# Optimization experiments

Hardware: AMD Instinct MI355X
Metric: run time of the kernel (lower is better)

The kernel has to match this reference:

```python
import jax, jax.numpy as jnp
import numpy as np

D_MODEL = 1024
NUM_HEADS = 16
HEAD_DIM = D_MODEL // NUM_HEADS


def setup_inputs() -> dict:
    key = jax.random.key(0)
    k1, k2, k3 = jax.random.split(key, 3)
    B, S = 2, 2048
    x = jax.random.normal(k1, (B, S, D_MODEL), dtype=jnp.float32)
    # torch nn.Linear weight layout: [out_features, in_features]
    qkv_w = jax.random.normal(k2, (3 * D_MODEL, D_MODEL), dtype=jnp.float32) * (D_MODEL ** -0.5)
    qkv_b = jnp.zeros((3 * D_MODEL,), dtype=jnp.float32)
    out_w = jax.random.normal(k3, (D_MODEL, D_MODEL), dtype=jnp.float32) * (D_MODEL ** -0.5)
    out_b = jnp.zeros((D_MODEL,), dtype=jnp.float32)
    return {"x": x, "qkv_w": qkv_w, "qkv_b": qkv_b, "out_w": out_w, "out_b": out_b}


def reference(x, qkv_w, qkv_b, out_w, out_b):
    B, S, D = x.shape
    H, hd = NUM_HEADS, HEAD_DIM
    # fused QKV projection (torch Linear: x @ W.T + b)
    qkv = jnp.dot(x, qkv_w.T) + qkv_b              # [B, S, 3D]
    qkv = qkv.reshape(B, S, 3, H, hd)
    qkv = jnp.transpose(qkv, (2, 0, 3, 1, 4))       # [3, B, H, S, hd]
    q, k, v = qkv[0], qkv[1], qkv[2]
    scale = hd ** -0.5
    scores = jnp.einsum('bhqd,bhkd->bhqk', q, k) * scale  # [B, H, S, S]
    # causal mask (TritonSoftmax(is_causal=True))
    causal = jnp.tril(jnp.ones((S, S), dtype=bool))
    scores = jnp.where(causal, scores, jnp.float32(-jnp.inf))
    attn = jax.nn.softmax(scores, axis=-1)
    ctx = jnp.einsum('bhqk,bhkd->bhqd', attn, v)    # [B, H, S, hd]
    ctx = jnp.transpose(ctx, (0, 2, 1, 3)).reshape(B, S, D)
    return jnp.dot(ctx, out_w.T) + out_b
```

## Files before the change

### kernel.cpp

```cpp
#include <hip/hip_runtime.h>

typedef unsigned short u16;
typedef __bf16 bf16x8 __attribute__((ext_vector_type(8)));
typedef float f32x4 __attribute__((ext_vector_type(4)));

#define LOG2E 1.44269504088896340736f

__device__ __forceinline__ u16 f2bf(float f) {
  unsigned int u = __builtin_bit_cast(unsigned int, f);
  u += 0x7FFFu + ((u >> 16) & 1u);
  return (u16)(u >> 16);
}

__device__ __forceinline__ unsigned int cvtpk_bf16(float lo, float hi) {
  unsigned int r;
  asm("v_cvt_pk_bf16_f32 %0, %1, %2" : "=v"(r) : "v"(lo), "v"(hi));
  return r;
}

__device__ __forceinline__ void async16(const void* g, void* l) {
  __builtin_amdgcn_global_load_lds((void*)g, (void*)l, 16, 0, 0);
}

__global__ void cast_all(const float* __restrict__ x, const float* __restrict__ w1,
                         const float* __restrict__ w2, u16* __restrict__ xb,
                         u16* __restrict__ w1b, u16* __restrict__ w2b) {
  int i = blockIdx.x * blockDim.x + threadIdx.x;
  const float* s; u16* d; int j;
  if (i < 1048576)      { s = x;  d = xb;  j = i; }
  else if (i < 1835008) { s = w1; d = w1b; j = i - 1048576; }
  else                  { s = w2; d = w2b; j = i - 1835008; }
  float4 v = ((const float4*)s)[j];
  union { u16 s4[4]; uint2 u; } o;
  o.s4[0] = f2bf(v.x); o.s4[1] = f2bf(v.y); o.s4[2] = f2bf(v.z); o.s4[3] = f2bf(v.w);
  ((uint2*)d)[j] = o.u;
}

template <int EPI, int BN>
__global__ __launch_bounds__(256)
void gemm_nt(const u16* __restrict__ A, const u16* __restrict__ Bw,
             int M, int N, int K, const float* __restrict__ bias,
             u16* __restrict__ qo, u16* __restrict__ ko, u16* __restrict__ vto,
             float* __restrict__ out, int ntn) {
  __shared__ __align__(16) u16 As[128 * 32];
  __shared__ __align__(16) u16 Bs[BN * 32];
  constexpr int JN = BN / 32;
  constexpr int NB = (BN * 4) / 256;
  const int tid = threadIdx.x;
  const int w = tid >> 6, lane = tid & 63;
  const int lr = lane & 15, lkb = lane >> 4;
  const int bx = blockIdx.x;
  const int mt = bx / ntn, nt = bx % ntn;
  const int m0 = mt * 128, n0 = nt * BN;
  const int wm = (w >> 1) * 64, wn = (w & 1) * (BN / 2);

  f32x4 acc[4][JN] = {};

  int srow[2], sgch[2];
#pragma unroll
  for (int i = 0; i < 2; ++i) {
    int cid = tid + i * 256;
    srow[i] = cid >> 2;
    sgch[i] = (cid & 3) ^ (srow[i] & 3);
  }

  for (int k0 = 0; k0 < K; k0 += 32) {
#pragma unroll
    for (int i = 0; i < 2; ++i) {
      char* la = (char*)As + (w * 64 + i * 256) * 16;
      async16(A + (size_t)(m0 + srow[i]) * K + k0 + sgch[i] * 8, la);
    }
#pragma unroll
    for (int i = 0; i < NB; ++i) {
      char* lb = (char*)Bs + (w * 64 + i * 256) * 16;
      async16(Bw + (size_t)(n0 + srow[i]) * K + k0 + sgch[i] * 8, lb);
    }
    __syncthreads();

    bf16x8 af[4], bfr[JN];
#pragma unroll
    for (int i = 0; i < 4; ++i) {
      int ra = wm + i * 16 + lr;
      af[i] = *(const bf16x8*)(As + ra * 32 + (lkb ^ (ra & 3)) * 8);
    }
#pragma unroll
    for (int j = 0; j < JN; ++j) {
      int rb = wn + j * 16 + lr;
      bfr[j] = *(const bf16x8*)(Bs + rb * 32 + (lkb ^ (rb & 3)) * 8);
    }
#pragma unroll
    for (int i = 0; i < 4; ++i)
#pragma unroll
      for (int j = 0; j < JN; ++j)
        acc[i][j] = __builtin_amdgcn_mfma_f32_16x16x32_bf16(af[i], bfr[j], acc[i][j], 0, 0, 0);
    __syncthreads();
  }

  if constexpr (EPI == 0) {
    const int which = n0 >> 10;
    const float qscale = (which == 0) ? 0.125f : 1.0f;
#pragma unroll
    for (int i = 0; i < 4; ++i) {
#pragma unroll
      for (int j = 0; j < JN; ++j) {
        int n = n0 + wn + j * 16 + lr;
        float bv = bias[n];
        int d = n & 1023, h = d >> 6, dd = d & 63;
#pragma unroll
        for (int r = 0; r < 4; ++r) {
          int m = m0 + wm + i * 16 + lkb * 4 + r;
          int b = m >> 11, s = m & 2047;
          int bh = b * 16 + h;
          u16 val = f2bf((acc[i][j][r] + bv) * qscale);
          if (which == 0)      qo[(bh * 2048 + s) * 64 + dd] = val;
          else if (which == 1) ko[(bh * 2048 + s) * 64 + dd] = val;
          else                 vto[(bh * 64 + dd) * 2048 + s] = val;
        }
      }
    }
  } else {
#pragma unroll
    for (int i = 0; i < 4; ++i)
#pragma unroll
      for (int j = 0; j < JN; ++j) {
        int n = n0 + wn + j * 16 + lr;
        float bv = bias[n];
#pragma unroll
        for (int r = 0; r < 4; ++r) {
          int m = m0 + wm + i * 16 + lkb * 4 + r;
          out[(size_t)m * N + n] = acc[i][j][r] + bv;
        }
      }
  }
}

__global__ __launch_bounds__(256)
void flash_attn(const u16* __restrict__ Q, const u16* __restrict__ Kg,
                const u16* __restrict__ Vt, u16* __restrict__ ctx) {
  __shared__ __align__(16) u16 Kls[2][64 * 64];
  __shared__ __align__(16) u16 Vls[2][64 * 64];
  const int tid = threadIdx.x;
  const int w = tid >> 6, lane = tid & 63;
  const int lr = lane & 15, lkb = lane >> 4;
  const int bid = blockIdx.x;
  const int qt = 31 - (bid >> 5);
  const int bh = bid & 31;
  const int q0 = qt * 64;
  const u16* Qh = Q + (size_t)bh * 2048 * 64;
  const u16* Kh = Kg + (size_t)bh * 2048 * 64;
  const u16* Vh = Vt + (size_t)bh * 2048 * 64;

  bf16x8 aQ[2];
#pragma unroll
  for (int kk = 0; kk < 2; ++kk)
    aQ[kk] = *(const bf16x8*)(Qh + (q0 + w * 16 + lr) * 64 + kk * 32 + lkb * 8);

  f32x4 acc[4] = {};
  float m_r = -1e30f, l_r = 0.f;

  int srow[2], sgch[2];
#pragma unroll
  for (int i = 0; i < 2; ++i) {
    int cid = tid + i * 256;
    srow[i] = cid >> 3;
    sgch[i] = (cid & 7) ^ (srow[i] & 7);
  }

  const int nkv = qt + 1;

  {
#pragma unroll
    for (int i = 0; i < 2; ++i) {
      char* lk = (char*)&Kls[0][0] + (w * 64 + i * 256) * 16;
      async16(Kh + (size_t)srow[i] * 64 + sgch[i] * 8, lk);
      char* lv = (char*)&Vls[0][0] + (w * 64 + i * 256) * 16;
      async16(Vh + (size_t)srow[i] * 2048 + sgch[i] * 8, lv);
    }
  }
  __syncthreads();

  for (int t = 0; t < nkv; ++t) {
    const int cur = t & 1;
    if (t + 1 < nkv) {
      const int kv1 = (t + 1) * 64;
#pragma unroll
      for (int i = 0; i < 2; ++i) {
        char* lk = (char*)&Kls[cur ^ 1][0] + (w * 64 + i * 256) * 16;
        async16(Kh + (size_t)(kv1 + srow[i]) * 64 + sgch[i] * 8, lk);
        char* lv = (char*)&Vls[cur ^ 1][0] + (w * 64 + i * 256) * 16;
        async16(Vh + (size_t)srow[i] * 2048 + kv1 + sgch[i] * 8, lv);
      }
    }
    const u16* Kb = &Kls[cur][0];
    const u16* Vb = &Vls[cur][0];

    f32x4 sc[4];
#pragma unroll
    for (int ct = 0; ct < 4; ++ct) {
      int row = ct * 16 + lr;
      int rs = row & 7;
      bf16x8 k0 = *(const bf16x8*)(Kb + row * 64 + (lkb ^ rs) * 8);
      bf16x8 k1 = *(const bf16x8*)(Kb + row * 64 + ((lkb + 4) ^ rs) * 8);
      f32x4 z = {};
      z = __builtin_amdgcn_mfma_f32_16x16x32_bf16(k0, aQ[0], z, 0, 0, 0);
      z = __builtin_amdgcn_mfma_f32_16x16x32_bf16(k1, aQ[1], z, 0, 0, 0);
      sc[ct] = z;
    }

    if (t == qt) {
#pragma unroll
      for (int ct = 0; ct < 4; ++ct)
#pragma unroll
        for (int r = 0; r < 4; ++r)
          if (ct * 16 + lkb * 4 + r > w * 16 + lr) sc[ct][r] = -1e30f;
    }

    float g0 = fmaxf(fmaxf(sc[0][0], sc[0][1]), fmaxf(sc[0][2], sc[0][3]));
    float g1 = fmaxf(fmaxf(sc[1][0], sc[1][1]), fmaxf(sc[1][2], sc[1][3]));
    float g2 = fmaxf(fmaxf(sc[2][0], sc[2][1]), fmaxf(sc[2][2], sc[2][3]));
    float g3 = fmaxf(fmaxf(sc[3][0], sc[3][1]), fmaxf(sc[3][2], sc[3][3]));
    float mt = fmaxf(fmaxf(g0, g1), fmaxf(g2, g3));
    mt = fmaxf(mt, __shfl_xor(mt, 16));
    mt = fmaxf(mt, __shfl_xor(mt, 32));

    if (!__all(mt <= m_r + 8.0f)) {
      float mnew = fmaxf(m_r, mt);
      float a = exp2f((m_r - mnew) * LOG2E);
      l_r *= a;
#pragma unroll
      for (int dt = 0; dt < 4; ++dt) acc[dt] *= a;
      m_r = mnew;
    }
    const float mls = m_r * LOG2E;
    float rsum = 0.f;
#pragma unroll
    for (int ct = 0; ct < 4; ++ct)
#pragma unroll
      for (int r = 0; r < 4; ++r) {
        float p = exp2f(__builtin_fmaf(sc[ct][r], LOG2E, -mls));
        sc[ct][r] = p;
        rsum += p;
      }
    rsum += __shfl_xor(rsum, 16);
    rsum += __shfl_xor(rsum, 32);
    l_r += rsum;

    unsigned int u[4][2];
#pragma unroll
    for (int ct = 0; ct < 4; ++ct) {
      u[ct][0] = cvtpk_bf16(sc[ct][0], sc[ct][1]);
      u[ct][1] = cvtpk_bf16(sc[ct][2], sc[ct][3]);
    }

    const int s0 = ((lkb & 1) << 5) + lr;
    const int s1 = s0 + 16;
    const int hi = lkb >> 1;
    bf16x8 Pf[2];
#pragma unroll
    for (int c = 0; c < 2; ++c) {
      const int c2 = c * 2;
      unsigned x0 = (unsigned)__shfl((int)u[c2][0], s0, 64);
      unsigned x1 = (unsigned)__shfl((int)u[c2][1], s0, 64);
      unsigned x2 = (unsigned)__shfl((int)u[c2][0], s1, 64);
      unsigned x3 = (unsigned)__shfl((int)u[c2][1], s1, 64);
      unsigned y0 = (unsigned)__shfl((int)u[c2 + 1][0], s0, 64);
      unsigned y1 = (unsigned)__shfl((int)u[c2 + 1][1], s0, 64);
      unsigned y2 = (unsigned)__shfl((int)u[c2 + 1][0], s1, 64);
      unsigned y3 = (unsigned)__shfl((int)u[c2 + 1][1], s1, 64);
      uint4 bb;
      bb.x = hi ? y0 : x0;
      bb.y = hi ? y1 : x1;
      bb.z = hi ? y2 : x2;
      bb.w = hi ? y3 : x3;
      Pf[c] = __builtin_bit_cast(bf16x8, bb);
    }

#pragma unroll
    for (int dt = 0; dt < 4; ++dt) {
      int row = dt * 16 + lr;
      int rs = row & 7;
      bf16x8 v0 = *(const bf16x8*)(Vb + row * 64 + (lkb ^ rs) * 8);
      bf16x8 v1 = *(const bf16x8*)(Vb + row * 64 + ((lkb + 4) ^ rs) * 8);
      acc[dt] = __builtin_amdgcn_mfma_f32_16x16x32_bf16(v0, Pf[0], acc[dt], 0, 0, 0);
      acc[dt] = __builtin_amdgcn_mfma_f32_16x16x32_bf16(v1, Pf[1], acc[dt], 0, 0, 0);
    }
    __syncthreads();
  }

  const float rl = 1.0f / l_r;
  const int b = bh >> 4, h = bh & 15;
  const int q = q0 + w * 16 + lr;
  const size_t base = ((size_t)(b * 2048 + q)) * 1024 + h * 64;
#pragma unroll
  for (int dt = 0; dt < 4; ++dt) {
    uint2 o;
    o.x = cvtpk_bf16(acc[dt][0] * rl, acc[dt][1] * rl);
    o.y = cvtpk_bf16(acc[dt][2] * rl, acc[dt][3] * rl);
    *(uint2*)(ctx + base + dt * 16 + lkb * 4) = o;
  }
}

extern "C" void kernel_launch(void* const* d_in, const int* in_sizes, int n_in,
                              void* d_out, int out_size, void* d_ws, size_t ws_size,
                              hipStream_t stream) {
  (void)in_sizes; (void)n_in; (void)out_size; (void)ws_size;
  const float* x = (const float*)d_in[0];
  const float* qkv_w = (const float*)d_in[1];
  const float* qkv_b = (const float*)d_in[2];
  const float* out_w = (const float*)d_in[3];
  const float* out_b = (const float*)d_in[4];
  float* out = (float*)d_out;

  char* ws = (char*)d_ws;
  u16* xb   = (u16*)(ws);
  u16* wqkv = (u16*)(ws + 8388608);
  u16* wout = (u16*)(ws + 14680064);
  u16* Qb   = (u16*)(ws + 16777216);
  u16* Kb   = (u16*)(ws + 25165824);
  u16* Vtb  = (u16*)(ws + 33554432);
  u16* ctx  = (u16*)(ws + 41943040);

  cast_all<<<8192, 256, 0, stream>>>(x, qkv_w, out_w, xb, wqkv, wout);

  gemm_nt<0, 128><<<768, 256, 0, stream>>>(xb, wqkv, 4096, 3072, 1024, qkv_b,
                                           Qb, Kb, Vtb, nullptr, 24);
  flash_attn<<<1024, 256, 0, stream>>>(Qb, Kb, Vtb, ctx);
  gemm_nt<1, 64><<<512, 256, 0, stream>>>(ctx, wout, 4096, 1024, 1024, out_b,
                                          nullptr, nullptr, nullptr, out, 16);
}
```

Measured before the change: 200.7 us.

## Restructure flash attention around 32x32x16 MFMA with 128-query tiles

Rewrites the attention kernel so each wave handles 32 query rows with 32x32x16 bf16 MFMAs, and each block covers 128 queries, halving the grid. The K/V shared-memory layout becomes chunk-major without the XOR swizzle. P-matrix transposition and row reductions use permlane32_swap instead of many shuffles. The change also adds s_setprio around the MFMA phases, a two-blocks-per-CU launch bound and interleaved long/short tile ordering for causal load balance. Software bf16 rounding replaces the packed convert instruction, which adds VALU work in the softmax and epilogue.

```diff
diff --git a/kernel.cpp b/kernel.cpp
--- a/kernel.cpp
+++ b/kernel.cpp
@@ -3,6 +3,8 @@
 typedef unsigned short u16;
 typedef __bf16 bf16x8 __attribute__((ext_vector_type(8)));
 typedef float f32x4 __attribute__((ext_vector_type(4)));
+typedef float f32x16 __attribute__((ext_vector_type(16)));
+typedef unsigned u32x2v __attribute__((ext_vector_type(2)));
 
 #define LOG2E 1.44269504088896340736f
 
@@ -12,10 +14,13 @@
   return (u16)(u >> 16);
 }
 
-__device__ __forceinline__ unsigned int cvtpk_bf16(float lo, float hi) {
-  unsigned int r;
-  asm("v_cvt_pk_bf16_f32 %0, %1, %2" : "=v"(r) : "v"(lo), "v"(hi));
-  return r;
+__device__ __forceinline__ unsigned pack2(float lo, float hi) {
+  return (unsigned)f2bf(lo) | ((unsigned)f2bf(hi) << 16);
+}
+
+__device__ __forceinline__ void pl32swap(unsigned& a, unsigned& b) {
+  u32x2v r = __builtin_amdgcn_permlane32_swap(a, b, false, false);
+  a = r[0]; b = r[1];
 }
 
 __device__ __forceinline__ void async16(const void* g, void* l) {
@@ -134,170 +139,162 @@
   }
 }
 
-__global__ __launch_bounds__(256)
+__global__ __launch_bounds__(256, 2)
 void flash_attn(const u16* __restrict__ Q, const u16* __restrict__ Kg,
                 const u16* __restrict__ Vt, u16* __restrict__ ctx) {
   __shared__ __align__(16) u16 Kls[2][64 * 64];
   __shared__ __align__(16) u16 Vls[2][64 * 64];
   const int tid = threadIdx.x;
   const int w = tid >> 6, lane = tid & 63;
-  const int lr = lane & 15, lkb = lane >> 4;
+  const int l5 = lane & 31, hi = lane >> 5;
   const int bid = blockIdx.x;
-  const int qt = 31 - (bid >> 5);
-  const int bh = bid & 31;
-  const int q0 = qt * 64;
-  const u16* Qh = Q + (size_t)bh * 2048 * 64;
-  const u16* Kh = Kg + (size_t)bh * 2048 * 64;
-  const u16* Vh = Vt + (size_t)bh * 2048 * 64;
-
-  bf16x8 aQ[2];
-#pragma unroll
-  for (int kk = 0; kk < 2; ++kk)
-    aQ[kk] = *(const bf16x8*)(Qh + (q0 + w * 16 + lr) * 64 + kk * 32 + lkb * 8);
-
-  f32x4 acc[4] = {};
+  const int h = bid & 31;
+  const int tt = bid >> 5;
+  const int qt = (tt < 8) ? (15 - tt) : (tt - 8);
+  const int q0w = qt * 128 + w * 32;
+  const int qrow = q0w + l5;
+  const u16* Qh = Q + (size_t)h * 2048 * 64;
+  const u16* Kh = Kg + (size_t)h * 2048 * 64;
+  const u16* Vh = Vt + (size_t)h * 2048 * 64;
+
+  bf16x8 bQ[4];
+#pragma unroll
+  for (int ks = 0; ks < 4; ++ks)
+    bQ[ks] = *(const bf16x8*)(Qh + (size_t)qrow * 64 + ks * 16 + hi * 8);
+
+  f32x16 accO[2] = {};
   float m_r = -1e30f, l_r = 0.f;
 
-  int srow[2], sgch[2];
-#pragma unroll
-  for (int i = 0; i < 2; ++i) {
-    int cid = tid + i * 256;
-    srow[i] = cid >> 3;
-    sgch[i] = (cid & 7) ^ (srow[i] & 7);
-  }
-
-  const int nkv = qt + 1;
-
-  {
-#pragma unroll
-    for (int i = 0; i < 2; ++i) {
-      char* lk = (char*)&Kls[0][0] + (w * 64 + i * 256) * 16;
-      async16(Kh + (size_t)srow[i] * 64 + sgch[i] * 8, lk);
-      char* lv = (char*)&Vls[0][0] + (w * 64 + i * 256) * 16;
-      async16(Vh + (size_t)srow[i] * 2048 + sgch[i] * 8, lv);
-    }
-  }
+  const int ra = tid & 63, ca = tid >> 6;
+  const int cb = ca + 4;
+  char* const ldA_K0 = (char*)&Kls[0][0] + (w * 64) * 16;
+  char* const ldB_K0 = (char*)&Kls[0][0] + (w * 64 + 256) * 16;
+  char* const ldA_V0 = (char*)&Vls[0][0] + (w * 64) * 16;
+  char* const ldB_V0 = (char*)&Vls[0][0] + (w * 64 + 256) * 16;
+  const int bufstep = 64 * 64 * 2;
+
+  const int nkv = 2 * qt + 2;
+
+  async16(Kh + (size_t)ra * 64 + ca * 8, ldA_K0);
+  async16(Kh + (size_t)ra * 64 + cb * 8, ldB_K0);
+  async16(Vh + (size_t)ra * 2048 + ca * 8, ldA_V0);
+  async16(Vh + (size_t)ra * 2048 + cb * 8, ldB_V0);
   __syncthreads();
 
   for (int t = 0; t < nkv; ++t) {
     const int cur = t & 1;
+    const int kv0 = t * 64;
     if (t + 1 < nkv) {
-      const int kv1 = (t + 1) * 64;
-#pragma unroll
-      for (int i = 0; i < 2; ++i) {
-        char* lk = (char*)&Kls[cur ^ 1][0] + (w * 64 + i * 256) * 16;
-        async16(Kh + (size_t)(kv1 + srow[i]) * 64 + sgch[i] * 8, lk);
-        char* lv = (char*)&Vls[cur ^ 1][0] + (w * 64 + i * 256) * 16;
-        async16(Vh + (size_t)srow[i] * 2048 + kv1 + sgch[i] * 8, lv);
-      }
-    }
-    const u16* Kb = &Kls[cur][0];
-    const u16* Vb = &Vls[cur][0];
-
-    f32x4 sc[4];
-#pragma unroll
-    for (int ct = 0; ct < 4; ++ct) {
-      int row = ct * 16 + lr;
-      int rs = row & 7;
-      bf16x8 k0 = *(const bf16x8*)(Kb + row * 64 + (lkb ^ rs) * 8);
-      bf16x8 k1 = *(const bf16x8*)(Kb + row * 64 + ((lkb + 4) ^ rs) * 8);
-      f32x4 z = {};
-      z = __builtin_amdgcn_mfma_f32_16x16x32_bf16(k0, aQ[0], z, 0, 0, 0);
-      z = __builtin_amdgcn_mfma_f32_16x16x32_bf16(k1, aQ[1], z, 0, 0, 0);
-      sc[ct] = z;
-    }
-
-    if (t == qt) {
-#pragma unroll
-      for (int ct = 0; ct < 4; ++ct)
-#pragma unroll
-        for (int r = 0; r < 4; ++r)
-          if (ct * 16 + lkb * 4 + r > w * 16 + lr) sc[ct][r] = -1e30f;
-    }
-
-    float g0 = fmaxf(fmaxf(sc[0][0], sc[0][1]), fmaxf(sc[0][2], sc[0][3]));
-    float g1 = fmaxf(fmaxf(sc[1][0], sc[1][1]), fmaxf(sc[1][2], sc[1][3]));
-    float g2 = fmaxf(fmaxf(sc[2][0], sc[2][1]), fmaxf(sc[2][2], sc[2][3]));
-    float g3 = fmaxf(fmaxf(sc[3][0], sc[3][1]), fmaxf(sc[3][2], sc[3][3]));
-    float mt = fmaxf(fmaxf(g0, g1), fmaxf(g2, g3));
-    mt = fmaxf(mt, __shfl_xor(mt, 16));
-    mt = fmaxf(mt, __shfl_xor(mt, 32));
-
-    if (!__all(mt <= m_r + 8.0f)) {
-      float mnew = fmaxf(m_r, mt);
-      float a = exp2f((m_r - mnew) * LOG2E);
-      l_r *= a;
-#pragma unroll
-      for (int dt = 0; dt < 4; ++dt) acc[dt] *= a;
-      m_r = mnew;
-    }
-    const float mls = m_r * LOG2E;
-    float rsum = 0.f;
-#pragma unroll
-    for (int ct = 0; ct < 4; ++ct)
-#pragma unroll
-      for (int r = 0; r < 4; ++r) {
-        float p = exp2f(__builtin_fmaf(sc[ct][r], LOG2E, -mls));
-        sc[ct][r] = p;
-        rsum += p;
-      }
-    rsum += __shfl_xor(rsum, 16);
-    rsum += __shfl_xor(rsum, 32);
-    l_r += rsum;
-
-    unsigned int u[4][2];
-#pragma unroll
-    for (int ct = 0; ct < 4; ++ct) {
-      u[ct][0] = cvtpk_bf16(sc[ct][0], sc[ct][1]);
-      u[ct][1] = cvtpk_bf16(sc[ct][2], sc[ct][3]);
-    }
-
-    const int s0 = ((lkb & 1) << 5) + lr;
-    const int s1 = s0 + 16;
-    const int hi = lkb >> 1;
-    bf16x8 Pf[2];
-#pragma unroll
-    for (int c = 0; c < 2; ++c) {
-      const int c2 = c * 2;
-      unsigned x0 = (unsigned)__shfl((int)u[c2][0], s0, 64);
-      unsigned x1 = (unsigned)__shfl((int)u[c2][1], s0, 64);
-      unsigned x2 = (unsigned)__shfl((int)u[c2][0], s1, 64);
-      unsigned x3 = (unsigned)__shfl((int)u[c2][1], s1, 64);
-      unsigned y0 = (unsigned)__shfl((int)u[c2 + 1][0], s0, 64);
-      unsigned y1 = (unsigned)__shfl((int)u[c2 + 1][1], s0, 64);
-      unsigned y2 = (unsigned)__shfl((int)u[c2 + 1][0], s1, 64);
-      unsigned y3 = (unsigned)__shfl((int)u[c2 + 1][1], s1, 64);
-      uint4 bb;
-      bb.x = hi ? y0 : x0;
-      bb.y = hi ? y1 : x1;
-      bb.z = hi ? y2 : x2;
-      bb.w = hi ? y3 : x3;
-      Pf[c] = __builtin_bit_cast(bf16x8, bb);
-    }
-
-#pragma unroll
-    for (int dt = 0; dt < 4; ++dt) {
-      int row = dt * 16 + lr;
-      int rs = row & 7;
-      bf16x8 v0 = *(const bf16x8*)(Vb + row * 64 + (lkb ^ rs) * 8);
-      bf16x8 v1 = *(const bf16x8*)(Vb + row * 64 + ((lkb + 4) ^ rs) * 8);
-      acc[dt] = __builtin_amdgcn_mfma_f32_16x16x32_bf16(v0, Pf[0], acc[dt], 0, 0, 0);
-      acc[dt] = __builtin_amdgcn_mfma_f32_16x16x32_bf16(v1, Pf[1], acc[dt], 0, 0, 0);
+      const int kv1 = kv0 + 64;
+      const int bo = (cur ^ 1) * bufstep;
+      async16(Kh + (size_t)(kv1 + ra) * 64 + ca * 8, ldA_K0 + bo);
+      async16(Kh + (size_t)(kv1 + ra) * 64 + cb * 8, ldB_K0 + bo);
+      async16(Vh + (size_t)ra * 2048 + kv1 + ca * 8, ldA_V0 + bo);
+      async16(Vh + (size_t)ra * 2048 + kv1 + cb * 8, ldB_V0 + bo);
+    }
+    if (kv0 <= q0w + 31) {
+      const u16* Kb = &Kls[cur][0];
+      const u16* Vb = &Vls[cur][0];
+
+      f32x16 sg[2];
+      __builtin_amdgcn_s_setprio(1);
+#pragma unroll
+      for (int g = 0; g < 2; ++g) {
+        f32x16 z = {};
+#pragma unroll
+        for (int ks = 0; ks < 4; ++ks) {
+          bf16x8 ka = *(const bf16x8*)(Kb + ((ks * 2 + hi) * 64 + g * 32 + l5) * 8);
+          z = __builtin_amdgcn_mfma_f32_32x32x16_bf16(ka, bQ[ks], z, 0, 0, 0);
+        }
+        sg[g] = z;
+      }
+      __builtin_amdgcn_s_setprio(0);
+
+      if (kv0 + 63 > q0w) {
+#pragma unroll
+        for (int g = 0; g < 2; ++g)
+#pragma unroll
+          for (int r = 0; r < 16; ++r) {
+            int kv = kv0 + g * 32 + (r & 3) + 8 * (r >> 2) + 4 * hi;
+            if (kv > qrow) sg[g][r] = -1e30f;
+          }
+      }
+
+      float mt = sg[0][0];
+#pragma unroll
+      for (int r = 1; r < 16; ++r) mt = fmaxf(mt, sg[0][r]);
+#pragma unroll
+      for (int r = 0; r < 16; ++r) mt = fmaxf(mt, sg[1][r]);
+      {
+        unsigned a = __builtin_bit_cast(unsigned, mt), b = a;
+        pl32swap(a, b);
+        mt = fmaxf(__builtin_bit_cast(float, a), __builtin_bit_cast(float, b));
+      }
+
+      if (!__all(mt <= m_r + 8.0f)) {
+        float mnew = fmaxf(m_r, mt);
+        float sca = exp2f((m_r - mnew) * LOG2E);
+        l_r *= sca;
+        accO[0] *= sca;
+        accO[1] *= sca;
+        m_r = mnew;
+      }
+      const float mls = m_r * LOG2E;
+      float rs = 0.f;
+#pragma unroll
+      for (int g = 0; g < 2; ++g)
+#pragma unroll
+        for (int r = 0; r < 16; ++r) {
+          float p = exp2f(__builtin_fmaf(sg[g][r], LOG2E, -mls));
+          sg[g][r] = p;
+          rs += p;
+        }
+      {
+        unsigned a = __builtin_bit_cast(unsigned, rs), b = a;
+        pl32swap(a, b);
+        rs = __builtin_bit_cast(float, a) + __builtin_bit_cast(float, b);
+      }
+      l_r += rs;
+
+      bf16x8 Pf[4];
+#pragma unroll
+      for (int s = 0; s < 4; ++s) {
+        const int g = s >> 1, b8 = (s & 1) * 8;
+        unsigned w0 = pack2(sg[g][b8 + 0], sg[g][b8 + 1]);
+        unsigned w1 = pack2(sg[g][b8 + 2], sg[g][b8 + 3]);
+        unsigned w2 = pack2(sg[g][b8 + 4], sg[g][b8 + 5]);
+        unsigned w3 = pack2(sg[g][b8 + 6], sg[g][b8 + 7]);
+        pl32swap(w0, w2);
+        pl32swap(w1, w3);
+        uint4 bb = {w0, w1, w2, w3};
+        Pf[s] = __builtin_bit_cast(bf16x8, bb);
+      }
+
+      __builtin_amdgcn_s_setprio(1);
+#pragma unroll
+      for (int g = 0; g < 2; ++g)
+#pragma unroll
+        for (int s = 0; s < 4; ++s) {
+          bf16x8 va = *(const bf16x8*)(Vb + ((s * 2 + hi) * 64 + g * 32 + l5) * 8);
+          accO[g] = __builtin_amdgcn_mfma_f32_32x32x16_bf16(va, Pf[s], accO[g], 0, 0, 0);
+        }
+      __builtin_amdgcn_s_setprio(0);
     }
     __syncthreads();
   }
 
   const float rl = 1.0f / l_r;
-  const int b = bh >> 4, h = bh & 15;
-  const int q = q0 + w * 16 + lr;
-  const size_t base = ((size_t)(b * 2048 + q)) * 1024 + h * 64;
-#pragma unroll
-  for (int dt = 0; dt < 4; ++dt) {
-    uint2 o;
-    o.x = cvtpk_bf16(acc[dt][0] * rl, acc[dt][1] * rl);
-    o.y = cvtpk_bf16(acc[dt][2] * rl, acc[dt][3] * rl);
-    *(uint2*)(ctx + base + dt * 16 + lkb * 4) = o;
-  }
+  const int b = h >> 4, hh = h & 15;
+  const size_t base = ((size_t)(b * 2048 + qrow)) * 1024 + hh * 64;
+#pragma unroll
+  for (int g = 0; g < 2; ++g)
+#pragma unroll
+    for (int qd = 0; qd < 4; ++qd) {
+      uint2 o;
+      o.x = pack2(accO[g][qd * 4 + 0] * rl, accO[g][qd * 4 + 1] * rl);
+      o.y = pack2(accO[g][qd * 4 + 2] * rl, accO[g][qd * 4 + 3] * rl);
+      *(uint2*)(ctx + base + g * 32 + qd * 8 + hi * 4) = o;
+    }
 }
 
 extern "C" void kernel_launch(void* const* d_in, const int* in_sizes, int n_in,
@@ -324,7 +321,7 @@
 
   gemm_nt<0, 128><<<768, 256, 0, stream>>>(xb, wqkv, 4096, 3072, 1024, qkv_b,
                                            Qb, Kb, Vtb, nullptr, 24);
-  flash_attn<<<1024, 256, 0, stream>>>(Qb, Kb, Vtb, ctx);
+  flash_attn<<<512, 256, 0, stream>>>(Qb, Kb, Vtb, ctx);
   gemm_nt<1, 64><<<512, 256, 0, stream>>>(ctx, wout, 4096, 1024, 1024, out_b,
                                           nullptr, nullptr, nullptr, out, 16);
 }
```

New measurement: 214.0 us. +6.6%, slower.
